# Performance work log

Measured on AMD Instinct MI355X. Metric: run time of the kernel, lower is better.

## Reference

```python
import jax, jax.numpy as jnp
import numpy as np
from jax import lax

B, HS, WS_, DIM = 4, 64, 64, 512
NH, WSZ = 8, 2
WH, SH, HD = 4, 4, 64        # wavelet heads, window heads, head_dim
WDIM, SDIM, RED = 256, 256, 64  # w_dim, s_dim, w_dim//4
SCALE = HD ** -0.5
EPS = 1e-5


def dwt_haar(x):
    # x: [B,C,H,W] -> [B,4C,H/2,W/2]; exact haar 2x2 stride-2 depthwise conv
    a = x[:, :, 0::2, 0::2]; b = x[:, :, 0::2, 1::2]
    c = x[:, :, 1::2, 0::2]; d = x[:, :, 1::2, 1::2]
    ll = 0.5 * (a + b + c + d)
    lh = 0.5 * (a + b - c - d)
    hl = 0.5 * (a - b + c - d)
    hh = 0.5 * (a - b - c + d)
    return jnp.concatenate([ll, lh, hl, hh], axis=1)


def idwt_haar(x):
    # x: [B,4C,h,w] -> [B,C,2h,2w]; exact haar conv_transpose stride 2
    Bx, C4, h, w = x.shape
    C = C4 // 4
    ll, lh, hl, hh = jnp.split(x, 4, axis=1)
    y00 = 0.5 * (ll + lh + hl + hh)
    y01 = 0.5 * (ll + lh - hl - hh)
    y10 = 0.5 * (ll - lh + hl - hh)
    y11 = 0.5 * (ll - lh - hl + hh)
    top = jnp.stack([y00, y01], axis=-1).reshape(Bx, C, h, 2 * w)
    bot = jnp.stack([y10, y11], axis=-1).reshape(Bx, C, h, 2 * w)
    return jnp.stack([top, bot], axis=-2).reshape(Bx, C, 2 * h, 2 * w)


def bn2d(x, g, b):
    # eval-mode BatchNorm2d with running_mean=0, running_var=1
    s = g / jnp.sqrt(1.0 + EPS)
    return x * s[None, :, None, None] + b[None, :, None, None]


def layernorm(x, g, b):
    m = jnp.mean(x, axis=-1, keepdims=True)
    v = jnp.var(x, axis=-1, keepdims=True)
    return (x - m) / jnp.sqrt(v + EPS) * g + b


def wsda_forward(x, wq_w, kv_ln_g, kv_ln_b, wkv_w, wkv_b, wproj_w, wproj_b,
                 reduce_w, reduce_b, reduce_bn_g, reduce_bn_b,
                 filter_w, filter_b, filter_bn_g, filter_bn_b,
                 sqkv_w, sproj_w, sproj_b, H, W):
    Bx, N, C = x.shape
    x4 = x.reshape(Bx, H, W, C)  # ws divides H,W -> no padding

    # ---- windowed attention branch (sa) ----
    hg, wg = H // WSZ, W // WSZ
    G, L = hg * wg, WSZ * WSZ
    xg = x4.reshape(Bx, hg, WSZ, wg, WSZ, C).transpose(0, 1, 3, 2, 4, 5).reshape(Bx, G, L, C)
    qkv = (xg @ sqkv_w).reshape(Bx, G, L, 3, SH, HD)
    q = qkv[:, :, :, 0].transpose(0, 1, 3, 2, 4)  # [B,G,SH,L,HD]
    k = qkv[:, :, :, 1].transpose(0, 1, 3, 2, 4)
    v = qkv[:, :, :, 2].transpose(0, 1, 3, 2, 4)
    attn = jax.nn.softmax(jnp.einsum('bghld,bghmd->bghlm', q, k) * SCALE, axis=-1)
    o = jnp.einsum('bghlm,bghmd->bghld', attn, v)
    o = o.transpose(0, 1, 3, 2, 4).reshape(Bx, hg, wg, WSZ, WSZ, SDIM)
    o = o.transpose(0, 1, 3, 2, 4, 5).reshape(Bx, H, W, SDIM)
    sa_out = o @ sproj_w + sproj_b

    # ---- wavelet attention branch (wa) ----
    q = (x4.reshape(Bx, N, C) @ wq_w).reshape(Bx, N, WH, HD).transpose(0, 2, 1, 3)  # [B,WH,N,HD]
    xc = x4.transpose(0, 3, 1, 2)  # NCHW
    r = jnp.einsum('bchw,co->bohw', xc, reduce_w) + reduce_b[None, :, None, None]
    r = jax.nn.relu(bn2d(r, reduce_bn_g, reduce_bn_b))          # [B,RED,H,W]
    xd = dwt_haar(r)                                            # [B,WDIM,H/2,W/2]
    f = lax.conv_general_dilated(xd, filter_w, (1, 1), 'SAME',
                                 dimension_numbers=('NCHW', 'OIHW', 'NCHW'))
    f = f + filter_b[None, :, None, None]
    xd = jax.nn.relu(bn2d(f, filter_bn_g, filter_bn_b))         # [B,WDIM,H/2,W/2]
    xi = idwt_haar(xd)                                          # [B,RED,H,W]
    x_idwt = xi.reshape(Bx, RED, H * W).transpose(0, 2, 1)      # [B,N,RED]
    kv_in = xd.reshape(Bx, WDIM, -1).transpose(0, 2, 1)         # [B,M,WDIM], M=(H/2)(W/2)
    kv_in = layernorm(kv_in, kv_ln_g, kv_ln_b)
    kv = (kv_in @ wkv_w + wkv_b).reshape(Bx, -1, 2, WH, HD)
    kk = kv[:, :, 0].transpose(0, 2, 1, 3)                      # [B,WH,M,HD]
    vv = kv[:, :, 1].transpose(0, 2, 1, 3)
    attn = jax.nn.softmax(jnp.einsum('bhnd,bhmd->bhnm', q, kk) * SCALE, axis=-1)
    ow = jnp.einsum('bhnm,bhmd->bhnd', attn, vv).transpose(0, 2, 1, 3).reshape(Bx, N, WDIM)
    wa_out = (jnp.concatenate([ow, x_idwt], axis=-1) @ wproj_w + wproj_b).reshape(Bx, H, W, WDIM)

    out = jnp.concatenate([sa_out, wa_out], axis=-1).reshape(Bx, N, C)
    return out


def setup_inputs() -> dict:
    key = jax.random.key(0)
    ks = jax.random.split(key, 10)
    w = lambda k, s: jax.random.normal(k, s, jnp.float32) * 0.02
    return {
        'x': jax.random.normal(ks[0], (B, HS * WS_, DIM), jnp.float32),
        'wq_w': w(ks[1], (DIM, WDIM)),
        'kv_ln_g': jnp.ones((WDIM,), jnp.float32),
        'kv_ln_b': jnp.zeros((WDIM,), jnp.float32),
        'wkv_w': w(ks[2], (WDIM, 2 * WDIM)),
        'wkv_b': jnp.zeros((2 * WDIM,), jnp.float32),
        'wproj_w': w(ks[3], (WDIM + RED, WDIM)),
        'wproj_b': jnp.zeros((WDIM,), jnp.float32),
        'reduce_w': w(ks[4], (DIM, RED)),
        'reduce_b': jnp.zeros((RED,), jnp.float32),
        'reduce_bn_g': jnp.ones((RED,), jnp.float32),
        'reduce_bn_b': jnp.zeros((RED,), jnp.float32),
        'filter_w': w(ks[5], (WDIM, WDIM, 3, 3)),
        'filter_b': jnp.zeros((WDIM,), jnp.float32),
        'filter_bn_g': jnp.ones((WDIM,), jnp.float32),
        'filter_bn_b': jnp.zeros((WDIM,), jnp.float32),
        'sqkv_w': w(ks[6], (DIM, 3 * SDIM)),
        'sproj_w': w(ks[7], (SDIM, SDIM)),
        'sproj_b': jnp.zeros((SDIM,), jnp.float32),
        'H': HS,
        'W': WS_,
    }


def reference(x, wq_w, kv_ln_g, kv_ln_b, wkv_w, wkv_b, wproj_w, wproj_b,
              reduce_w, reduce_b, reduce_bn_g, reduce_bn_b,
              filter_w, filter_b, filter_bn_g, filter_bn_b,
              sqkv_w, sproj_w, sproj_b, H, W):
    return wsda_forward(x, wq_w, kv_ln_g, kv_ln_b, wkv_w, wkv_b, wproj_w, wproj_b,
                        reduce_w, reduce_b, reduce_bn_g, reduce_bn_b,
                        filter_w, filter_b, filter_bn_g, filter_bn_b,
                        sqkv_w, sproj_w, sproj_b, H, W)
```

## Files before the change

kernel.cpp:

```cpp
#include <hip/hip_runtime.h>
#include <hip/hip_bf16.h>
#include <math.h>

#define WEPS 1e-5f
#define WSCALE 0.125f
#define QSCALE 0.1803368801111244f

enum { EPI_NONE=0, EPI_BIAS=1, EPI_BN_RELU=2 };

typedef __attribute__((ext_vector_type(8))) short bf16x8;
typedef __attribute__((ext_vector_type(4))) float f32x4;

static __device__ inline unsigned short f2bf(float f) {
    __hip_bfloat16 h = __float2bfloat16(f);
    return *(unsigned short*)&h;
}
static __device__ inline float exp2_fast(float x) {
    float r;
    asm("v_exp_f32 %0, %1" : "=v"(r) : "v"(x));
    return r;
}
static __device__ inline unsigned cvt_pk_bf16(float a, float b) {
    unsigned r;
    asm("v_cvt_pk_bf16_f32 %0, %1, %2" : "=v"(r) : "v"(a), "v"(b));
    return r;
}
static __device__ inline int xcd_swizzle_id() {
    int id = blockIdx.x;
    int q = gridDim.x >> 3;
    return (id & 7) * q + (id >> 3);
}

static __device__ inline bf16x8 lds_frag(const unsigned short* base, int row, int inner) {
    int byte = row * 128 + (inner ^ ((row & 7) << 4));
    return *(const bf16x8*)((const char*)base + byte);
}
static __device__ inline bf16x8 lds_frag256(const unsigned short* base, int row, int inner) {
    int byte = row * 256 + (inner ^ ((row & 15) << 4));
    return *(const bf16x8*)((const char*)base + byte);
}

template<int EPI, int OBF16>
__launch_bounds__(256)
__global__ void gemm_bf16(const __hip_bfloat16* __restrict__ A, int lda,
                          const __hip_bfloat16* __restrict__ Bt, int K,
                          void* __restrict__ Cv, int ldc, int N, int nbx,
                          const float* __restrict__ bias,
                          const float* __restrict__ bn_g,
                          const float* __restrict__ bn_b,
                          float oscale)
{
    __shared__ unsigned short As[8192];
    __shared__ unsigned short Bs[8192];
    const int tid = threadIdx.x;
    const int lane = tid & 63, wv = tid >> 6;
    const int g = lane >> 4, l16 = lane & 15;
    const int wr = wv >> 1, wc = wv & 1;
    const int w = xcd_swizzle_id();
    const int bm = (w / nbx) << 7;
    const int bn = (w % nbx) << 7;
    f32x4 acc[4][4];
    #pragma unroll
    for (int i = 0; i < 4; i++)
        #pragma unroll
        for (int j = 0; j < 4; j++)
            #pragma unroll
            for (int r = 0; r < 4; r++) acc[i][j][r] = 0.f;

    for (int k0 = 0; k0 < K; k0 += 64) {
        __syncthreads();
        #pragma unroll
        for (int it = 0; it < 4; it++) {
            int idx = tid + (it << 8);
            int row = idx >> 3, seg = idx & 7;
            int wb = row * 128 + ((seg << 4) ^ ((row & 7) << 4));
            float4 av = *(const float4*)(A + (size_t)(bm + row) * lda + k0 + (seg << 3));
            *(float4*)((char*)As + wb) = av;
            int col = bn + row;
            float4 bv = make_float4(0.f,0.f,0.f,0.f);
            if (col < N) bv = *(const float4*)(Bt + (size_t)col * K + k0 + (seg << 3));
            *(float4*)((char*)Bs + wb) = bv;
        }
        __syncthreads();
        #pragma unroll
        for (int ks = 0; ks < 2; ks++) {
            bf16x8 af[4], bfr[4];
            #pragma unroll
            for (int i = 0; i < 4; i++)
                af[i] = lds_frag(As, (wr<<6) + (i<<4) + l16, (ks<<6) + (g<<4));
            #pragma unroll
            for (int j = 0; j < 4; j++)
                bfr[j] = lds_frag(Bs, (wc<<6) + (j<<4) + l16, (ks<<6) + (g<<4));
            #pragma unroll
            for (int i = 0; i < 4; i++)
                #pragma unroll
                for (int j = 0; j < 4; j++)
                    acc[i][j] = __builtin_amdgcn_mfma_f32_16x16x32_bf16(af[i], bfr[j], acc[i][j], 0, 0, 0);
        }
    }
    const float bn_s = 0.99999500003749968f;
    #pragma unroll
    for (int i = 0; i < 4; i++) {
        int m = bm + (wr<<6) + (i<<4) + (g<<2);
        #pragma unroll
        for (int j = 0; j < 4; j++) {
            int c = bn + (wc<<6) + (j<<4) + l16;
            if (c >= N) continue;
            float bi = (EPI != EPI_NONE) ? bias[c] : 0.f;
            float sc = 1.f, bb = 0.f;
            if (EPI == EPI_BN_RELU) { sc = bn_g[c] * bn_s; bb = bn_b[c]; }
            #pragma unroll
            for (int r = 0; r < 4; r++) {
                float t = acc[i][j][r] * oscale + bi;
                if (EPI == EPI_BN_RELU) t = fmaxf(t * sc + bb, 0.f);
                if (OBF16) ((__hip_bfloat16*)Cv)[(size_t)(m+r)*ldc + c] = __float2bfloat16(t);
                else       ((float*)Cv)[(size_t)(m+r)*ldc + c] = t;
            }
        }
    }
}

__launch_bounds__(256)
__global__ void gemmX(const __hip_bfloat16* __restrict__ A,
                      const __hip_bfloat16* __restrict__ Bt,
                      __hip_bfloat16* __restrict__ qkvb,
                      __hip_bfloat16* __restrict__ qbw,
                      float* __restrict__ rbuf,
                      const float* __restrict__ red_b,
                      const float* __restrict__ rbn_g,
                      const float* __restrict__ rbn_b)
{
    __shared__ unsigned short As[8192];
    __shared__ unsigned short Bs[8192];
    const int tid = threadIdx.x;
    const int lane = tid & 63, wv = tid >> 6;
    const int g = lane >> 4, l16 = lane & 15;
    const int wr = wv >> 1, wc = wv & 1;
    const int w = xcd_swizzle_id();
    const int bm = (w / 9) << 7;
    const int bn = (w % 9) << 7;
    f32x4 acc[4][4];
    #pragma unroll
    for (int i = 0; i < 4; i++)
        #pragma unroll
        for (int j = 0; j < 4; j++)
            #pragma unroll
            for (int r = 0; r < 4; r++) acc[i][j][r] = 0.f;

    for (int k0 = 0; k0 < 512; k0 += 64) {
        __syncthreads();
        #pragma unroll
        for (int it = 0; it < 4; it++) {
            int idx = tid + (it << 8);
            int row = idx >> 3, seg = idx & 7;
            int wb = row * 128 + ((seg << 4) ^ ((row & 7) << 4));
            float4 av = *(const float4*)(A + (size_t)(bm + row) * 512 + k0 + (seg << 3));
            *(float4*)((char*)As + wb) = av;
            int col = bn + row;
            float4 bv = make_float4(0.f,0.f,0.f,0.f);
            if (col < 1088) bv = *(const float4*)(Bt + (size_t)col * 512 + k0 + (seg << 3));
            *(float4*)((char*)Bs + wb) = bv;
        }
        __syncthreads();
        #pragma unroll
        for (int ks = 0; ks < 2; ks++) {
            bf16x8 af[4], bfr[4];
            #pragma unroll
            for (int i = 0; i < 4; i++)
                af[i] = lds_frag(As, (wr<<6) + (i<<4) + l16, (ks<<6) + (g<<4));
            #pragma unroll
            for (int j = 0; j < 4; j++)
                bfr[j] = lds_frag(Bs, (wc<<6) + (j<<4) + l16, (ks<<6) + (g<<4));
            #pragma unroll
            for (int i = 0; i < 4; i++)
                #pragma unroll
                for (int j = 0; j < 4; j++)
                    acc[i][j] = __builtin_amdgcn_mfma_f32_16x16x32_bf16(af[i], bfr[j], acc[i][j], 0, 0, 0);
        }
    }
    const float bn_s = 0.99999500003749968f;
    #pragma unroll
    for (int i = 0; i < 4; i++) {
        int m = bm + (wr<<6) + (i<<4) + (g<<2);
        #pragma unroll
        for (int j = 0; j < 4; j++) {
            int c = bn + (wc<<6) + (j<<4) + l16;
            if (c >= 1088) continue;
            if (c < 768) {
                #pragma unroll
                for (int r = 0; r < 4; r++)
                    qkvb[(size_t)(m+r)*768 + c] = __float2bfloat16(acc[i][j][r]);
            } else if (c < 1024) {
                int c2 = c - 768;
                #pragma unroll
                for (int r = 0; r < 4; r++)
                    qbw[(size_t)(m+r)*256 + c2] = __float2bfloat16(acc[i][j][r] * QSCALE);
            } else {
                int c2 = c - 1024;
                float sc = rbn_g[c2] * bn_s, bb = rbn_b[c2], bi = red_b[c2];
                #pragma unroll
                for (int r = 0; r < 4; r++)
                    rbuf[(size_t)(m+r)*64 + c2] = fmaxf((acc[i][j][r] + bi) * sc + bb, 0.f);
            }
        }
    }
}

__launch_bounds__(256)
__global__ void gemm64_kv(const __hip_bfloat16* __restrict__ A,
                          const __hip_bfloat16* __restrict__ Bt,
                          __hip_bfloat16* __restrict__ kbo,
                          __hip_bfloat16* __restrict__ vto,
                          const float* __restrict__ bias)
{
    __shared__ unsigned short As[2][4096];
    __shared__ unsigned short Bs[2][4096];
    const int tid = threadIdx.x;
    const int lane = tid & 63, wv = tid >> 6;
    const int g = lane >> 4, l16 = lane & 15;
    const int wr = wv >> 1, wc = wv & 1;
    const int bm = blockIdx.y << 6;
    const int bn = blockIdx.x << 6;

    int swb[2];
    const __hip_bfloat16 *Ap[2], *Bp[2];
    #pragma unroll
    for (int it = 0; it < 2; it++) {
        int idx = tid + (it << 8);
        int row = idx >> 3, seg = idx & 7;
        swb[it] = row * 128 + ((seg << 4) ^ ((row & 7) << 4));
        Ap[it] = A  + (size_t)(bm + row) * 256 + (seg << 3);
        Bp[it] = Bt + (size_t)(bn + row) * 256 + (seg << 3);
    }
    f32x4 acc[2][2];
    #pragma unroll
    for (int i = 0; i < 2; i++)
        #pragma unroll
        for (int j = 0; j < 2; j++)
            #pragma unroll
            for (int r = 0; r < 4; r++) acc[i][j][r] = 0.f;

    #pragma unroll
    for (int it = 0; it < 2; it++) {
        *(float4*)((char*)As[0] + swb[it]) = *(const float4*)(Ap[it]);
        *(float4*)((char*)Bs[0] + swb[it]) = *(const float4*)(Bp[it]);
    }
    __syncthreads();

    int cur = 0;
    for (int t = 0; t < 4; t++) {
        float4 ra[2], rb[2];
        const bool has_next = (t < 3);
        if (has_next) {
            #pragma unroll
            for (int it = 0; it < 2; it++) {
                ra[it] = *(const float4*)(Ap[it] + ((t + 1) << 6));
                rb[it] = *(const float4*)(Bp[it] + ((t + 1) << 6));
            }
        }
        #pragma unroll
        for (int ks = 0; ks < 2; ks++) {
            bf16x8 af[2], bfr[2];
            #pragma unroll
            for (int i = 0; i < 2; i++)
                af[i] = lds_frag(As[cur], (wr<<5) + (i<<4) + l16, (ks<<6) + (g<<4));
            #pragma unroll
            for (int j = 0; j < 2; j++)
                bfr[j] = lds_frag(Bs[cur], (wc<<5) + (j<<4) + l16, (ks<<6) + (g<<4));
            #pragma unroll
            for (int i = 0; i < 2; i++)
                #pragma unroll
                for (int j = 0; j < 2; j++)
                    acc[i][j] = __builtin_amdgcn_mfma_f32_16x16x32_bf16(af[i], bfr[j], acc[i][j], 0, 0, 0);
        }
        if (has_next) {
            #pragma unroll
            for (int it = 0; it < 2; it++) {
                *(float4*)((char*)As[cur^1] + swb[it]) = ra[it];
                *(float4*)((char*)Bs[cur^1] + swb[it]) = rb[it];
            }
        }
        __syncthreads();
        cur ^= 1;
    }

    #pragma unroll
    for (int i = 0; i < 2; i++) {
        int m = bm + (wr<<5) + (i<<4) + (g<<2);
        int bimg = m >> 10, tkn0 = m & 1023;
        #pragma unroll
        for (int j = 0; j < 2; j++) {
            int c = bn + (wc<<5) + (j<<4) + l16;
            if (c < 256) {
                int wh = c >> 6, d0 = c & 63;
                __hip_bfloat16* kp = kbo + (((size_t)((bimg<<2)+wh)) << 16) + (size_t)tkn0*64 + d0;
                #pragma unroll
                for (int r = 0; r < 4; r++)
                    kp[r*64] = __float2bfloat16(acc[i][j][r] + bias[c]);
            } else {
                int c2 = c - 256;
                int wh = c2 >> 6, d = c2 & 63;
                float bi = bias[256 + c2];
                ushort4 h;
                h.x = f2bf(acc[i][j][0] + bi);
                h.y = f2bf(acc[i][j][1] + bi);
                h.z = f2bf(acc[i][j][2] + bi);
                h.w = f2bf(acc[i][j][3] + bi);
                *(ushort4*)(vto + (((size_t)((bimg<<2)+wh)) << 16) + (size_t)d*1024 + tkn0) = h;
            }
        }
    }
}

__launch_bounds__(256)
__global__ void gemm_wproj(const __hip_bfloat16* __restrict__ A1,
                           const __hip_bfloat16* __restrict__ A2,
                           const __hip_bfloat16* __restrict__ Bt,
                           float* __restrict__ C,
                           const float* __restrict__ bias)
{
    __shared__ unsigned short As[8192];
    __shared__ unsigned short Bs[8192];
    const int tid = threadIdx.x;
    const int lane = tid & 63, wv = tid >> 6;
    const int g = lane >> 4, l16 = lane & 15;
    const int wr = wv >> 1, wc = wv & 1;
    const int w = xcd_swizzle_id();
    const int bm = (w >> 1) << 7;
    const int bn = (w & 1) << 7;
    f32x4 acc[4][4];
    #pragma unroll
    for (int i = 0; i < 4; i++)
        #pragma unroll
        for (int j = 0; j < 4; j++)
            #pragma unroll
            for (int r = 0; r < 4; r++) acc[i][j][r] = 0.f;

    for (int k0 = 0; k0 < 320; k0 += 64) {
        __syncthreads();
        #pragma unroll
        for (int it = 0; it < 4; it++) {
            int idx = tid + (it << 8);
            int row = idx >> 3, seg = idx & 7;
            int wb = row * 128 + ((seg << 4) ^ ((row & 7) << 4));
            float4 av;
            if (k0 < 256)
                av = *(const float4*)(A1 + (size_t)(bm + row) * 256 + k0 + (seg << 3));
            else
                av = *(const float4*)(A2 + (size_t)(bm + row) * 64 + (k0 - 256) + (seg << 3));
            *(float4*)((char*)As + wb) = av;
            float4 bv = *(const float4*)(Bt + (size_t)(bn + row) * 320 + k0 + (seg << 3));
            *(float4*)((char*)Bs + wb) = bv;
        }
        __syncthreads();
        #pragma unroll
        for (int ks = 0; ks < 2; ks++) {
            bf16x8 af[4], bfr[4];
            #pragma unroll
            for (int i = 0; i < 4; i++)
                af[i] = lds_frag(As, (wr<<6) + (i<<4) + l16, (ks<<6) + (g<<4));
            #pragma unroll
            for (int j = 0; j < 4; j++)
                bfr[j] = lds_frag(Bs, (wc<<6) + (j<<4) + l16, (ks<<6) + (g<<4));
            #pragma unroll
            for (int i = 0; i < 4; i++)
                #pragma unroll
                for (int j = 0; j < 4; j++)
                    acc[i][j] = __builtin_amdgcn_mfma_f32_16x16x32_bf16(af[i], bfr[j], acc[i][j], 0, 0, 0);
        }
    }
    #pragma unroll
    for (int i = 0; i < 4; i++) {
        int m = bm + (wr<<6) + (i<<4) + (g<<2);
        #pragma unroll
        for (int j = 0; j < 4; j++) {
            int c = bn + (wc<<6) + (j<<4) + l16;
            float bi = bias[c];
            #pragma unroll
            for (int r = 0; r < 4; r++)
                C[(size_t)(m+r)*512 + c] = acc[i][j][r] + bi;
        }
    }
}

__launch_bounds__(256)
__global__ void conv3_mfma(const __hip_bfloat16* __restrict__ Xd,
                           const __hip_bfloat16* __restrict__ Wt,
                           float* __restrict__ C,
                           const float* __restrict__ bias,
                           const float* __restrict__ bn_g,
                           const float* __restrict__ bn_b)
{
    __shared__ unsigned short As[2][8192];
    __shared__ unsigned short Bs[2][8192];
    const int tid = threadIdx.x;
    const int lane = tid & 63, wv = tid >> 6;
    const int g = lane >> 4, l16 = lane & 15;
    const int wr = wv >> 1, wc = wv & 1;
    const int bm = blockIdx.y << 6;
    const int bn = blockIdx.x << 6;

    int srow[4], sseg[4], swb[4];
    #pragma unroll
    for (int it = 0; it < 4; it++) {
        int idx = tid + (it << 8);
        srow[it] = idx >> 4;
        sseg[it] = idx & 15;
        swb[it]  = srow[it] * 256 + ((sseg[it] << 4) ^ ((srow[it] & 15) << 4));
    }
    int abase[4], ay[4], ax[4];
    #pragma unroll
    for (int it = 0; it < 4; it++) {
        int m = bm + srow[it];
        int bimg = m >> 10, s = m & 1023;
        ay[it] = s >> 5; ax[it] = s & 31;
        abase[it] = bimg << 10;
    }

    f32x4 acc[2][2];
    #pragma unroll
    for (int i = 0; i < 2; i++)
        #pragma unroll
        for (int j = 0; j < 2; j++)
            #pragma unroll
            for (int r = 0; r < 4; r++) acc[i][j][r] = 0.f;

    #pragma unroll
    for (int it = 0; it < 4; it++) {
        int y = ay[it] - 1, xx = ax[it] - 1;
        float4 av = make_float4(0.f,0.f,0.f,0.f);
        if ((unsigned)y < 32u && (unsigned)xx < 32u)
            av = *(const float4*)(Xd + ((size_t)(abase[it] + (y<<5) + xx) << 8) + (sseg[it] << 3));
        *(float4*)((char*)As[0] + swb[it]) = av;
        float4 bv = *(const float4*)(Wt + (size_t)(bn + srow[it]) * 2304 + (sseg[it] << 3));
        *(float4*)((char*)Bs[0] + swb[it]) = bv;
    }
    __syncthreads();

    int cur = 0;
    for (int t = 0; t < 18; t++) {
        float4 ra[4], rb[4];
        const bool has_next = (t + 1 < 18);
        if (has_next) {
            int tn = t + 1;
            int tap = tn >> 1;
            int dy = tap / 3 - 1;
            int dx = tap - (tap / 3) * 3 - 1;
            int i0 = (tn & 1) << 7;
            #pragma unroll
            for (int it = 0; it < 4; it++) {
                int y = ay[it] + dy, xx = ax[it] + dx;
                ra[it] = make_float4(0.f,0.f,0.f,0.f);
                if ((unsigned)y < 32u && (unsigned)xx < 32u)
                    ra[it] = *(const float4*)(Xd + ((size_t)(abase[it] + (y<<5) + xx) << 8) + i0 + (sseg[it] << 3));
                rb[it] = *(const float4*)(Wt + (size_t)(bn + srow[it]) * 2304 + tn * 128 + (sseg[it] << 3));
            }
        }
        #pragma unroll
        for (int ks = 0; ks < 4; ks++) {
            bf16x8 af[2], bfr[2];
            #pragma unroll
            for (int i = 0; i < 2; i++)
                af[i] = lds_frag256(As[cur], (wr<<5) + (i<<4) + l16, (ks<<6) + (g<<4));
            #pragma unroll
            for (int j = 0; j < 2; j++)
                bfr[j] = lds_frag256(Bs[cur], (wc<<5) + (j<<4) + l16, (ks<<6) + (g<<4));
            #pragma unroll
            for (int i = 0; i < 2; i++)
                #pragma unroll
                for (int j = 0; j < 2; j++)
                    acc[i][j] = __builtin_amdgcn_mfma_f32_16x16x32_bf16(af[i], bfr[j], acc[i][j], 0, 0, 0);
        }
        if (has_next) {
            #pragma unroll
            for (int it = 0; it < 4; it++) {
                *(float4*)((char*)As[cur^1] + swb[it]) = ra[it];
                *(float4*)((char*)Bs[cur^1] + swb[it]) = rb[it];
            }
        }
        __syncthreads();
        cur ^= 1;
    }

    const float bn_s = 0.99999500003749968f;
    #pragma unroll
    for (int i = 0; i < 2; i++) {
        int m = bm + (wr<<5) + (i<<4) + (g<<2);
        #pragma unroll
        for (int j = 0; j < 2; j++) {
            int c = bn + (wc<<5) + (j<<4) + l16;
            float sc = bn_g[c] * bn_s, bb = bn_b[c], bi = bias[c];
            #pragma unroll
            for (int r = 0; r < 4; r++)
                C[(size_t)(m + r) * 256 + c] = fmaxf((acc[i][j][r] + bi) * sc + bb, 0.f);
        }
    }
}

static __device__ inline void tr_task(const float* in, __hip_bfloat16* o,
                                      int K, int N, int nb, int tid)
{
    int idx = nb * 256 + tid;
    int n = idx / K, k = idx - n * K;
    o[idx] = __float2bfloat16(in[(size_t)k * N + n]);
}

__global__ void prep_all(const float* __restrict__ x,
                         const float* __restrict__ sqkv_w, const float* __restrict__ wq_w,
                         const float* __restrict__ reduce_w, const float* __restrict__ sproj_w,
                         const float* __restrict__ wkv_w, const float* __restrict__ wproj_w,
                         const float* __restrict__ filter_w,
                         __hip_bfloat16* __restrict__ xb, __hip_bfloat16* __restrict__ sqkvT,
                         __hip_bfloat16* __restrict__ wqT, __hip_bfloat16* __restrict__ redT,
                         __hip_bfloat16* __restrict__ sprojT, __hip_bfloat16* __restrict__ wkvT,
                         __hip_bfloat16* __restrict__ wprojT, __hip_bfloat16* __restrict__ wt2b)
{
    int bid = blockIdx.x, tid = threadIdx.x;
    if (bid < 8192) {
        int i = bid * 256 + tid;
        float4 v = ((const float4*)x)[i];
        ushort4 h;
        h.x = f2bf(v.x); h.y = f2bf(v.y); h.z = f2bf(v.z); h.w = f2bf(v.w);
        *(ushort4*)(xb + (size_t)i * 4) = h;
        return;
    }
    bid -= 8192;
    if (bid < 1536) { tr_task(sqkv_w, sqkvT, 512, 768, bid, tid); return; }
    bid -= 1536;
    if (bid < 512)  { tr_task(wq_w, wqT, 512, 256, bid, tid); return; }
    bid -= 512;
    if (bid < 128)  { tr_task(reduce_w, redT, 512, 64, bid, tid); return; }
    bid -= 128;
    if (bid < 256)  { tr_task(sproj_w, sprojT, 256, 256, bid, tid); return; }
    bid -= 256;
    if (bid < 512)  { tr_task(wkv_w, wkvT, 256, 512, bid, tid); return; }
    bid -= 512;
    if (bid < 320)  { tr_task(wproj_w, wprojT, 320, 256, bid, tid); return; }
    bid -= 320;
    {
        int oc = bid;
        const float* src = filter_w + (size_t)(oc * 256 + tid) * 9;
        __hip_bfloat16* dst = wt2b + (size_t)oc * 2304 + tid;
        #pragma unroll
        for (int tap = 0; tap < 9; tap++)
            dst[tap * 256] = __float2bfloat16(src[tap]);
    }
}

__launch_bounds__(256)
__global__ void win_attn(const __hip_bfloat16* __restrict__ qkv,
                         __hip_bfloat16* __restrict__ sa_o)
{
    int gw = blockIdx.x * 4 + (threadIdx.x >> 6);
    int lane = threadIdx.x & 63;
    int b  = gw >> 12;
    int g  = (gw >> 2) & 1023;
    int sh = gw & 3;
    int hg = g >> 5, wg = g & 31;
    float q[4], k[4], v[4];
    int rows[4];
    #pragma unroll
    for (int l = 0; l < 4; l++) {
        int h = (hg << 1) + (l >> 1), w = (wg << 1) + (l & 1);
        int row = (b << 12) + (h << 6) + w;
        rows[l] = row;
        const __hip_bfloat16* p = qkv + (size_t)row * 768 + sh * 64 + lane;
        q[l] = __bfloat162float(p[0]);
        k[l] = __bfloat162float(p[256]);
        v[l] = __bfloat162float(p[512]);
    }
    float s[4][4];
    #pragma unroll
    for (int l = 0; l < 4; l++)
        #pragma unroll
        for (int m = 0; m < 4; m++) s[l][m] = q[l] * k[m];
    #pragma unroll
    for (int off = 32; off > 0; off >>= 1)
        #pragma unroll
        for (int l = 0; l < 4; l++)
            #pragma unroll
            for (int m = 0; m < 4; m++)
                s[l][m] += __shfl_xor(s[l][m], off, 64);
    #pragma unroll
    for (int l = 0; l < 4; l++) {
        float s0 = s[l][0]*WSCALE, s1 = s[l][1]*WSCALE, s2 = s[l][2]*WSCALE, s3 = s[l][3]*WSCALE;
        float mx = fmaxf(fmaxf(s0,s1), fmaxf(s2,s3));
        float p0 = __expf(s0-mx), p1 = __expf(s1-mx), p2 = __expf(s2-mx), p3 = __expf(s3-mx);
        float inv = 1.f / (p0+p1+p2+p3);
        float o = (p0*v[0] + p1*v[1] + p2*v[2] + p3*v[3]) * inv;
        sa_o[(size_t)rows[l] * 256 + sh * 64 + lane] = __float2bfloat16(o);
    }
}

__global__ void dwt_kernel(const float* __restrict__ r, __hip_bfloat16* __restrict__ xd)
{
    int t = blockIdx.x * 256 + threadIdx.x;
    int o = t & 63;
    int x = (t >> 6) & 31;
    int y = (t >> 11) & 31;
    int b = t >> 16;
    const float* rb = r + (b << 18);
    int base = ((y << 1) << 6) + (x << 1);
    float a  = rb[(base     ) * 64 + o];
    float bb = rb[(base +  1) * 64 + o];
    float c  = rb[(base + 64) * 64 + o];
    float d  = rb[(base + 65) * 64 + o];
    float ll = 0.5f*(a+bb+c+d), lh = 0.5f*(a+bb-c-d);
    float hl = 0.5f*(a-bb+c-d), hh = 0.5f*(a-bb-c+d);
    __hip_bfloat16* outp = xd + (((b << 10) + (y << 5) + x) << 8) + o;
    outp[0]   = __float2bfloat16(ll);
    outp[64]  = __float2bfloat16(lh);
    outp[128] = __float2bfloat16(hl);
    outp[192] = __float2bfloat16(hh);
}

__launch_bounds__(256)
__global__ void ln_idwt(const float* __restrict__ X, const float* __restrict__ g,
                        const float* __restrict__ bta, __hip_bfloat16* __restrict__ Y,
                        __hip_bfloat16* __restrict__ xi)
{
    int bid = blockIdx.x;
    int t = threadIdx.x;
    if (bid < 4096) {
        int row = bid;
        float x = X[(size_t)row * 256 + t];
        __shared__ float red[4];
        int wv = t >> 6, ln = t & 63;
        float s = x;
        #pragma unroll
        for (int off = 32; off > 0; off >>= 1) s += __shfl_xor(s, off, 64);
        if (ln == 0) red[wv] = s;
        __syncthreads();
        float m = (red[0]+red[1]+red[2]+red[3]) * (1.f/256.f);
        float d = x - m;
        float s2 = d * d;
        #pragma unroll
        for (int off = 32; off > 0; off >>= 1) s2 += __shfl_xor(s2, off, 64);
        __syncthreads();
        if (ln == 0) red[wv] = s2;
        __syncthreads();
        float var = (red[0]+red[1]+red[2]+red[3]) * (1.f/256.f);
        float inv = 1.f / sqrtf(var + WEPS);
        Y[(size_t)row * 256 + t] = __float2bfloat16(d * inv * g[t] + bta[t]);
        return;
    }
    int tt = (bid - 4096) * 256 + t;
    int o = tt & 63;
    int x = (tt >> 6) & 31;
    int y = (tt >> 11) & 31;
    int b = tt >> 16;
    const float* p = X + (((b << 10) + (y << 5) + x) << 8);
    float ll = p[o], lh = p[64+o], hl = p[128+o], hh = p[192+o];
    float y00 = 0.5f*(ll+lh+hl+hh);
    float y01 = 0.5f*(ll+lh-hl-hh);
    float y10 = 0.5f*(ll-lh+hl-hh);
    float y11 = 0.5f*(ll-lh-hl+hh);
    __hip_bfloat16* ob = xi + ((size_t)b << 18);
    int base = ((y << 1) << 6) + (x << 1);
    ob[(size_t)(base     ) * 64 + o] = __float2bfloat16(y00);
    ob[(size_t)(base +  1) * 64 + o] = __float2bfloat16(y01);
    ob[(size_t)(base + 64) * 64 + o] = __float2bfloat16(y10);
    ob[(size_t)(base + 65) * 64 + o] = __float2bfloat16(y11);
}

__launch_bounds__(256)
__global__ void flash_mfma(const __hip_bfloat16* __restrict__ qb,
                           const __hip_bfloat16* __restrict__ kb,
                           const __hip_bfloat16* __restrict__ vt,
                           __hip_bfloat16* __restrict__ ow)
{
    __shared__ unsigned short Ks[4096];
    __shared__ unsigned short Vs[4096];
    const int tid = threadIdx.x;
    const int wv = tid >> 6;
    const int lane = tid & 63;
    const int g = lane >> 4, q16 = lane & 15;
    const int bh = blockIdx.y;
    const int b = bh >> 2, wh = bh & 3;
    const int qbase = (blockIdx.x << 6) + (wv << 4);

    const __hip_bfloat16* qp = qb + ((size_t)((b << 12) + qbase + q16)) * 256 + wh * 64 + g * 8;
    bf16x8 qf0 = *(const bf16x8*)qp;
    bf16x8 qf1 = *(const bf16x8*)(qp + 32);

    const __hip_bfloat16* kbase = kb + ((size_t)bh << 16);
    const __hip_bfloat16* vbase = vt + ((size_t)bh << 16);

    f32x4 oacc[4];
    #pragma unroll
    for (int dc = 0; dc < 4; dc++)
        #pragma unroll
        for (int r = 0; r < 4; r++) oacc[dc][r] = 0.f;
    float m_cur = -1e30f;
    float lsum_part = 0.f;

    for (int t0 = 0; t0 < 1024; t0 += 64) {
        __syncthreads();
        #pragma unroll
        for (int it = 0; it < 2; it++) {
            int off = (tid << 4) + (it << 12);
            int row = off >> 7;
            int inner = off & 127;
            int wb = row * 128 + (inner ^ ((row & 7) << 4));
            float4 kd = *(const float4*)(kbase + (t0 + row) * 64 + (inner >> 1));
            float4 vd = *(const float4*)(vbase + row * 1024 + t0 + (inner >> 1));
            *(float4*)((char*)Ks + wb) = kd;
            *(float4*)((char*)Vs + wb) = vd;
        }
        __syncthreads();

        f32x4 st[4];
        __builtin_amdgcn_s_setprio(1);
        #pragma unroll
        for (int sub = 0; sub < 4; sub++) {
            #pragma unroll
            for (int r = 0; r < 4; r++) st[sub][r] = 0.f;
            bf16x8 k0 = lds_frag(Ks, sub * 16 + q16, g * 16);
            bf16x8 k1 = lds_frag(Ks, sub * 16 + q16, 64 + g * 16);
            st[sub] = __builtin_amdgcn_mfma_f32_16x16x32_bf16(k0, qf0, st[sub], 0, 0, 0);
            st[sub] = __builtin_amdgcn_mfma_f32_16x16x32_bf16(k1, qf1, st[sub], 0, 0, 0);
        }
        __builtin_amdgcn_s_setprio(0);

        float pmax = -1e30f;
        #pragma unroll
        for (int t = 0; t < 4; t++)
            #pragma unroll
            for (int r = 0; r < 4; r++) pmax = fmaxf(pmax, st[t][r]);
        if (!__all(pmax <= m_cur + 11.5f)) {
            float mx = pmax;
            mx = fmaxf(mx, __shfl_xor(mx, 16, 64));
            mx = fmaxf(mx, __shfl_xor(mx, 32, 64));
            float m_new = fmaxf(m_cur, mx);
            float alpha = exp2_fast(m_cur - m_new);
            lsum_part *= alpha;
            #pragma unroll
            for (int r = 0; r < 4; r++) {
                float sc = __shfl(alpha, (g << 2) + r, 64);
                #pragma unroll
                for (int dc = 0; dc < 4; dc++) oacc[dc][r] *= sc;
            }
            m_cur = m_new;
        }

        float psum = 0.f;
        unsigned pk[4][2];
        #pragma unroll
        for (int t = 0; t < 4; t++) {
            float p0 = exp2_fast(st[t][0] - m_cur), p1 = exp2_fast(st[t][1] - m_cur);
            float p2 = exp2_fast(st[t][2] - m_cur), p3 = exp2_fast(st[t][3] - m_cur);
            psum += (p0 + p1) + (p2 + p3);
            pk[t][0] = cvt_pk_bf16(p0, p1);
            pk[t][1] = cvt_pk_bf16(p2, p3);
        }
        lsum_part += psum;

        bool ghi = (g & 2) != 0;
        unsigned pkA0[2], pkA1[2];
        pkA0[0] = ghi ? pk[1][0] : pk[0][0];
        pkA0[1] = ghi ? pk[1][1] : pk[0][1];
        pkA1[0] = ghi ? pk[3][0] : pk[2][0];
        pkA1[1] = ghi ? pk[3][1] : pk[2][1];
        union { int u[4]; bf16x8 v; } A0, A1;
        #pragma unroll
        for (int c = 0; c < 4; c++) {
            int src = (((2 * g + (c >> 1)) & 3) << 4) | q16;
            A0.u[c] = __shfl((int)pkA0[c & 1], src, 64);
            A1.u[c] = __shfl((int)pkA1[c & 1], src, 64);
        }

        __builtin_amdgcn_s_setprio(1);
        #pragma unroll
        for (int dc = 0; dc < 4; dc++) {
            bf16x8 v0 = lds_frag(Vs, dc * 16 + q16, g * 16);
            bf16x8 v1 = lds_frag(Vs, dc * 16 + q16, 64 + g * 16);
            oacc[dc] = __builtin_amdgcn_mfma_f32_16x16x32_bf16(A0.v, v0, oacc[dc], 0, 0, 0);
            oacc[dc] = __builtin_amdgcn_mfma_f32_16x16x32_bf16(A1.v, v1, oacc[dc], 0, 0, 0);
        }
        __builtin_amdgcn_s_setprio(0);
    }

    lsum_part += __shfl_xor(lsum_part, 16, 64);
    lsum_part += __shfl_xor(lsum_part, 32, 64);
    #pragma unroll
    for (int r = 0; r < 4; r++) {
        float inv = 1.f / __shfl(lsum_part, (g << 2) + r, 64);
        int qrow = (b << 12) + qbase + (g << 2) + r;
        #pragma unroll
        for (int dc = 0; dc < 4; dc++)
            ow[(size_t)qrow * 256 + wh * 64 + dc * 16 + q16] =
                __float2bfloat16(oacc[dc][r] * inv);
    }
}

extern "C" void kernel_launch(void* const* d_in, const int* in_sizes, int n_in,
                              void* d_out, int out_size, void* d_ws, size_t ws_size,
                              hipStream_t stream)
{
    const float* x        = (const float*)d_in[0];
    const float* wq_w     = (const float*)d_in[1];
    const float* kv_ln_g  = (const float*)d_in[2];
    const float* kv_ln_b  = (const float*)d_in[3];
    const float* wkv_w    = (const float*)d_in[4];
    const float* wkv_b    = (const float*)d_in[5];
    const float* wproj_w  = (const float*)d_in[6];
    const float* wproj_b  = (const float*)d_in[7];
    const float* reduce_w = (const float*)d_in[8];
    const float* reduce_b = (const float*)d_in[9];
    const float* rbn_g    = (const float*)d_in[10];
    const float* rbn_b    = (const float*)d_in[11];
    const float* filter_w = (const float*)d_in[12];
    const float* filter_b = (const float*)d_in[13];
    const float* fbn_g    = (const float*)d_in[14];
    const float* fbn_b    = (const float*)d_in[15];
    const float* sqkv_w   = (const float*)d_in[16];
    const float* sproj_w  = (const float*)d_in[17];
    const float* sproj_b  = (const float*)d_in[18];
    float* out = (float*)d_out;
    float* ws  = (float*)d_ws;

    __hip_bfloat16* qkvb  = (__hip_bfloat16*)(ws);
    __hip_bfloat16* owb   = (__hip_bfloat16*)(ws);
    __hip_bfloat16* sa_ob = (__hip_bfloat16*)(ws + 6291456);
    __hip_bfloat16* xb    = (__hip_bfloat16*)(ws + 8388608);
    __hip_bfloat16* sqkvT = (__hip_bfloat16*)(ws + 12582912);
    __hip_bfloat16* wqT   = (__hip_bfloat16*)(ws + 12779520);
    __hip_bfloat16* redT  = (__hip_bfloat16*)(ws + 12845056);
    __hip_bfloat16* sprojT= (__hip_bfloat16*)(ws + 12861440);
    __hip_bfloat16* wkvT  = (__hip_bfloat16*)(ws + 12894208);
    __hip_bfloat16* wprojT= (__hip_bfloat16*)(ws + 13025280);
    __hip_bfloat16* wt2b  = (__hip_bfloat16*)(ws + 13066240);
    float* rbuf  = ws + 13361152;
    __hip_bfloat16* xd1b  = (__hip_bfloat16*)(ws + 14409728);
    float* xd2   = ws + 14934016;
    __hip_bfloat16* kvinb = (__hip_bfloat16*)(ws + 15982592);
    __hip_bfloat16* xidwtb= (__hip_bfloat16*)(ws + 16506880);
    __hip_bfloat16* qbw   = (__hip_bfloat16*)(ws + 17031168);
    __hip_bfloat16* kbb   = (__hip_bfloat16*)(ws + 19128320);
    __hip_bfloat16* vtb   = (__hip_bfloat16*)(ws + 19652608);

    dim3 blk(256);

    prep_all<<<dim3(11712), blk, 0, stream>>>(x, sqkv_w, wq_w, reduce_w, sproj_w,
                                              wkv_w, wproj_w, filter_w,
                                              xb, sqkvT, wqT, redT, sprojT, wkvT,
                                              wprojT, wt2b);

    gemmX<<<dim3(1152), blk, 0, stream>>>(xb, sqkvT, qkvb, qbw, rbuf,
                                          reduce_b, rbn_g, rbn_b);
    win_attn<<<dim3(4096), blk, 0, stream>>>(qkvb, sa_ob);
    gemm_bf16<EPI_BIAS,0><<<dim3(256), blk, 0, stream>>>(sa_ob, 256, sprojT, 256, out, 512,
                                                         256, 2, sproj_b, nullptr, nullptr, 1.f);
    dwt_kernel<<<dim3(1024), blk, 0, stream>>>(rbuf, xd1b);
    conv3_mfma<<<dim3(4,64), blk, 0, stream>>>(xd1b, wt2b, xd2, filter_b, fbn_g, fbn_b);
    ln_idwt<<<dim3(5120), blk, 0, stream>>>(xd2, kv_ln_g, kv_ln_b, kvinb, xidwtb);
    gemm64_kv<<<dim3(8,64), blk, 0, stream>>>(kvinb, wkvT, kbb, vtb, wkv_b);
    flash_mfma<<<dim3(64,16), blk, 0, stream>>>(qbw, kbb, vtb, owb);
    gemm_wproj<<<dim3(256), blk, 0, stream>>>(owb, xidwtb, wprojT, out + 256, wproj_b);
}
```

Before: 177.8 us.

## Double-buffer LDS tiles with register prefetch in three GEMM kernels

Converts the generic GEMM, the fused QKV GEMM and the wproj GEMM from single-buffered LDS staging to a double-buffered ping-pong scheme. The next K-tile is loaded from global memory into registers before the MFMA loop over the current tile, then written to the other LDS buffer, which removes one barrier per iteration and lets global load latency overlap compute. Per-thread address math is also hoisted out of the loop. The cost is doubled LDS use (64KB per block) and more live registers, which may reduce occupancy.

```diff
diff --git a/kernel.cpp b/kernel.cpp
--- a/kernel.cpp
+++ b/kernel.cpp
@@ -50,8 +50,8 @@
                           const float* __restrict__ bn_b,
                           float oscale)
 {
-    __shared__ unsigned short As[8192];
-    __shared__ unsigned short Bs[8192];
+    __shared__ unsigned short As[2][8192];
+    __shared__ unsigned short Bs[2][8192];
     const int tid = threadIdx.x;
     const int lane = tid & 63, wv = tid >> 6;
     const int g = lane >> 4, l16 = lane & 15;
@@ -59,6 +59,20 @@
     const int w = xcd_swizzle_id();
     const int bm = (w / nbx) << 7;
     const int bn = (w % nbx) << 7;
+
+    int swb[4];
+    const __hip_bfloat16 *Ap[4], *Bp[4];
+    bool bok[4];
+    #pragma unroll
+    for (int it = 0; it < 4; it++) {
+        int idx = tid + (it << 8);
+        int row = idx >> 3, seg = idx & 7;
+        swb[it] = row * 128 + ((seg << 4) ^ ((row & 7) << 4));
+        Ap[it] = A + (size_t)(bm + row) * lda + (seg << 3);
+        int col = bn + row;
+        bok[it] = col < N;
+        Bp[it] = Bt + (size_t)(bok[it] ? col : 0) * K + (seg << 3);
+    }
     f32x4 acc[4][4];
     #pragma unroll
     for (int i = 0; i < 4; i++)
@@ -67,36 +81,53 @@
             #pragma unroll
             for (int r = 0; r < 4; r++) acc[i][j][r] = 0.f;
 
-    for (int k0 = 0; k0 < K; k0 += 64) {
-        __syncthreads();
-        #pragma unroll
-        for (int it = 0; it < 4; it++) {
-            int idx = tid + (it << 8);
-            int row = idx >> 3, seg = idx & 7;
-            int wb = row * 128 + ((seg << 4) ^ ((row & 7) << 4));
-            float4 av = *(const float4*)(A + (size_t)(bm + row) * lda + k0 + (seg << 3));
-            *(float4*)((char*)As + wb) = av;
-            int col = bn + row;
-            float4 bv = make_float4(0.f,0.f,0.f,0.f);
-            if (col < N) bv = *(const float4*)(Bt + (size_t)col * K + k0 + (seg << 3));
-            *(float4*)((char*)Bs + wb) = bv;
-        }
-        __syncthreads();
+    #pragma unroll
+    for (int it = 0; it < 4; it++) {
+        *(float4*)((char*)As[0] + swb[it]) = *(const float4*)(Ap[it]);
+        float4 bv = make_float4(0.f,0.f,0.f,0.f);
+        if (bok[it]) bv = *(const float4*)(Bp[it]);
+        *(float4*)((char*)Bs[0] + swb[it]) = bv;
+    }
+    __syncthreads();
+
+    int cur = 0;
+    const int niter = K >> 6;
+    for (int t = 0; t < niter; t++) {
+        float4 ra[4], rb[4];
+        const bool has_next = (t + 1 < niter);
+        if (has_next) {
+            int kb = (t + 1) << 6;
+            #pragma unroll
+            for (int it = 0; it < 4; it++) {
+                ra[it] = *(const float4*)(Ap[it] + kb);
+                rb[it] = make_float4(0.f,0.f,0.f,0.f);
+                if (bok[it]) rb[it] = *(const float4*)(Bp[it] + kb);
+            }
+        }
         #pragma unroll
         for (int ks = 0; ks < 2; ks++) {
             bf16x8 af[4], bfr[4];
             #pragma unroll
             for (int i = 0; i < 4; i++)
-                af[i] = lds_frag(As, (wr<<6) + (i<<4) + l16, (ks<<6) + (g<<4));
+                af[i] = lds_frag(As[cur], (wr<<6) + (i<<4) + l16, (ks<<6) + (g<<4));
             #pragma unroll
             for (int j = 0; j < 4; j++)
-                bfr[j] = lds_frag(Bs, (wc<<6) + (j<<4) + l16, (ks<<6) + (g<<4));
+                bfr[j] = lds_frag(Bs[cur], (wc<<6) + (j<<4) + l16, (ks<<6) + (g<<4));
             #pragma unroll
             for (int i = 0; i < 4; i++)
                 #pragma unroll
                 for (int j = 0; j < 4; j++)
                     acc[i][j] = __builtin_amdgcn_mfma_f32_16x16x32_bf16(af[i], bfr[j], acc[i][j], 0, 0, 0);
         }
+        if (has_next) {
+            #pragma unroll
+            for (int it = 0; it < 4; it++) {
+                *(float4*)((char*)As[cur^1] + swb[it]) = ra[it];
+                *(float4*)((char*)Bs[cur^1] + swb[it]) = rb[it];
+            }
+        }
+        __syncthreads();
+        cur ^= 1;
     }
     const float bn_s = 0.99999500003749968f;
     #pragma unroll
@@ -130,8 +161,8 @@
                       const float* __restrict__ rbn_g,
                       const float* __restrict__ rbn_b)
 {
-    __shared__ unsigned short As[8192];
-    __shared__ unsigned short Bs[8192];
+    __shared__ unsigned short As[2][8192];
+    __shared__ unsigned short Bs[2][8192];
     const int tid = threadIdx.x;
     const int lane = tid & 63, wv = tid >> 6;
     const int g = lane >> 4, l16 = lane & 15;
@@ -139,6 +170,20 @@
     const int w = xcd_swizzle_id();
     const int bm = (w / 9) << 7;
     const int bn = (w % 9) << 7;
+
+    int swb[4];
+    const __hip_bfloat16 *Ap[4], *Bp[4];
+    bool bok[4];
+    #pragma unroll
+    for (int it = 0; it < 4; it++) {
+        int idx = tid + (it << 8);
+        int row = idx >> 3, seg = idx & 7;
+        swb[it] = row * 128 + ((seg << 4) ^ ((row & 7) << 4));
+        Ap[it] = A + (size_t)(bm + row) * 512 + (seg << 3);
+        int col = bn + row;
+        bok[it] = col < 1088;
+        Bp[it] = Bt + (size_t)(bok[it] ? col : 0) * 512 + (seg << 3);
+    }
     f32x4 acc[4][4];
     #pragma unroll
     for (int i = 0; i < 4; i++)
@@ -147,36 +192,52 @@
             #pragma unroll
             for (int r = 0; r < 4; r++) acc[i][j][r] = 0.f;
 
-    for (int k0 = 0; k0 < 512; k0 += 64) {
-        __syncthreads();
-        #pragma unroll
-        for (int it = 0; it < 4; it++) {
-            int idx = tid + (it << 8);
-            int row = idx >> 3, seg = idx & 7;
-            int wb = row * 128 + ((seg << 4) ^ ((row & 7) << 4));
-            float4 av = *(const float4*)(A + (size_t)(bm + row) * 512 + k0 + (seg << 3));
-            *(float4*)((char*)As + wb) = av;
-            int col = bn + row;
-            float4 bv = make_float4(0.f,0.f,0.f,0.f);
-            if (col < 1088) bv = *(const float4*)(Bt + (size_t)col * 512 + k0 + (seg << 3));
-            *(float4*)((char*)Bs + wb) = bv;
-        }
-        __syncthreads();
+    #pragma unroll
+    for (int it = 0; it < 4; it++) {
+        *(float4*)((char*)As[0] + swb[it]) = *(const float4*)(Ap[it]);
+        float4 bv = make_float4(0.f,0.f,0.f,0.f);
+        if (bok[it]) bv = *(const float4*)(Bp[it]);
+        *(float4*)((char*)Bs[0] + swb[it]) = bv;
+    }
+    __syncthreads();
+
+    int cur = 0;
+    for (int t = 0; t < 8; t++) {
+        float4 ra[4], rb[4];
+        const bool has_next = (t < 7);
+        if (has_next) {
+            int kb = (t + 1) << 6;
+            #pragma unroll
+            for (int it = 0; it < 4; it++) {
+                ra[it] = *(const float4*)(Ap[it] + kb);
+                rb[it] = make_float4(0.f,0.f,0.f,0.f);
+                if (bok[it]) rb[it] = *(const float4*)(Bp[it] + kb);
+            }
+        }
         #pragma unroll
         for (int ks = 0; ks < 2; ks++) {
             bf16x8 af[4], bfr[4];
             #pragma unroll
             for (int i = 0; i < 4; i++)
-                af[i] = lds_frag(As, (wr<<6) + (i<<4) + l16, (ks<<6) + (g<<4));
+                af[i] = lds_frag(As[cur], (wr<<6) + (i<<4) + l16, (ks<<6) + (g<<4));
             #pragma unroll
             for (int j = 0; j < 4; j++)
-                bfr[j] = lds_frag(Bs, (wc<<6) + (j<<4) + l16, (ks<<6) + (g<<4));
+                bfr[j] = lds_frag(Bs[cur], (wc<<6) + (j<<4) + l16, (ks<<6) + (g<<4));
             #pragma unroll
             for (int i = 0; i < 4; i++)
                 #pragma unroll
                 for (int j = 0; j < 4; j++)
                     acc[i][j] = __builtin_amdgcn_mfma_f32_16x16x32_bf16(af[i], bfr[j], acc[i][j], 0, 0, 0);
         }
+        if (has_next) {
+            #pragma unroll
+            for (int it = 0; it < 4; it++) {
+                *(float4*)((char*)As[cur^1] + swb[it]) = ra[it];
+                *(float4*)((char*)Bs[cur^1] + swb[it]) = rb[it];
+            }
+        }
+        __syncthreads();
+        cur ^= 1;
     }
     const float bn_s = 0.99999500003749968f;
     #pragma unroll
@@ -319,8 +380,8 @@
                            float* __restrict__ C,
                            const float* __restrict__ bias)
 {
-    __shared__ unsigned short As[8192];
-    __shared__ unsigned short Bs[8192];
+    __shared__ unsigned short As[2][8192];
+    __shared__ unsigned short Bs[2][8192];
     const int tid = threadIdx.x;
     const int lane = tid & 63, wv = tid >> 6;
     const int g = lane >> 4, l16 = lane & 15;
@@ -328,6 +389,16 @@
     const int w = xcd_swizzle_id();
     const int bm = (w >> 1) << 7;
     const int bn = (w & 1) << 7;
+
+    int srow[4], sseg[4], swb[4];
+    const __hip_bfloat16 *Bp[4];
+    #pragma unroll
+    for (int it = 0; it < 4; it++) {
+        int idx = tid + (it << 8);
+        srow[it] = idx >> 3; sseg[it] = idx & 7;
+        swb[it] = srow[it] * 128 + ((sseg[it] << 4) ^ ((srow[it] & 7) << 4));
+        Bp[it] = Bt + (size_t)(bn + srow[it]) * 320 + (sseg[it] << 3);
+    }
     f32x4 acc[4][4];
     #pragma unroll
     for (int i = 0; i < 4; i++)
@@ -336,38 +407,53 @@
             #pragma unroll
             for (int r = 0; r < 4; r++) acc[i][j][r] = 0.f;
 
-    for (int k0 = 0; k0 < 320; k0 += 64) {
-        __syncthreads();
-        #pragma unroll
-        for (int it = 0; it < 4; it++) {
-            int idx = tid + (it << 8);
-            int row = idx >> 3, seg = idx & 7;
-            int wb = row * 128 + ((seg << 4) ^ ((row & 7) << 4));
-            float4 av;
-            if (k0 < 256)
-                av = *(const float4*)(A1 + (size_t)(bm + row) * 256 + k0 + (seg << 3));
-            else
-                av = *(const float4*)(A2 + (size_t)(bm + row) * 64 + (k0 - 256) + (seg << 3));
-            *(float4*)((char*)As + wb) = av;
-            float4 bv = *(const float4*)(Bt + (size_t)(bn + row) * 320 + k0 + (seg << 3));
-            *(float4*)((char*)Bs + wb) = bv;
-        }
-        __syncthreads();
+    #pragma unroll
+    for (int it = 0; it < 4; it++) {
+        *(float4*)((char*)As[0] + swb[it]) =
+            *(const float4*)(A1 + (size_t)(bm + srow[it]) * 256 + (sseg[it] << 3));
+        *(float4*)((char*)Bs[0] + swb[it]) = *(const float4*)(Bp[it]);
+    }
+    __syncthreads();
+
+    int cur = 0;
+    for (int t = 0; t < 5; t++) {
+        float4 ra[4], rb[4];
+        const bool has_next = (t < 4);
+        if (has_next) {
+            int kb = (t + 1) << 6;
+            #pragma unroll
+            for (int it = 0; it < 4; it++) {
+                if (kb < 256)
+                    ra[it] = *(const float4*)(A1 + (size_t)(bm + srow[it]) * 256 + kb + (sseg[it] << 3));
+                else
+                    ra[it] = *(const float4*)(A2 + (size_t)(bm + srow[it]) * 64 + (kb - 256) + (sseg[it] << 3));
+                rb[it] = *(const float4*)(Bp[it] + kb);
+            }
+        }
         #pragma unroll
         for (int ks = 0; ks < 2; ks++) {
             bf16x8 af[4], bfr[4];
             #pragma unroll
             for (int i = 0; i < 4; i++)
-                af[i] = lds_frag(As, (wr<<6) + (i<<4) + l16, (ks<<6) + (g<<4));
+                af[i] = lds_frag(As[cur], (wr<<6) + (i<<4) + l16, (ks<<6) + (g<<4));
             #pragma unroll
             for (int j = 0; j < 4; j++)
-                bfr[j] = lds_frag(Bs, (wc<<6) + (j<<4) + l16, (ks<<6) + (g<<4));
+                bfr[j] = lds_frag(Bs[cur], (wc<<6) + (j<<4) + l16, (ks<<6) + (g<<4));
             #pragma unroll
             for (int i = 0; i < 4; i++)
                 #pragma unroll
                 for (int j = 0; j < 4; j++)
                     acc[i][j] = __builtin_amdgcn_mfma_f32_16x16x32_bf16(af[i], bfr[j], acc[i][j], 0, 0, 0);
         }
+        if (has_next) {
+            #pragma unroll
+            for (int it = 0; it < 4; it++) {
+                *(float4*)((char*)As[cur^1] + swb[it]) = ra[it];
+                *(float4*)((char*)Bs[cur^1] + swb[it]) = rb[it];
+            }
+        }
+        __syncthreads();
+        cur ^= 1;
     }
     #pragma unroll
     for (int i = 0; i < 4; i++) {
```

Measured after the change: 207.3 us. +16.6%, slower.

## Double-buffer shared memory tiles in gemmX with register prefetch

Applied to the files above, without the earlier changes.

The input projection GEMM now uses two LDS buffers for A and B. The next K-tile is prefetched into registers while MFMAs run on the current tile, then written into the alternate buffer, which leaves one barrier per iteration instead of two. Global load addresses are precomputed once. The aim is to hide global memory latency behind compute, at the cost of doubled LDS use (64KB) and more registers, which may reduce occupancy.

```diff
diff --git a/kernel.cpp b/kernel.cpp
--- a/kernel.cpp
+++ b/kernel.cpp
@@ -130,8 +130,8 @@
                       const float* __restrict__ rbn_g,
                       const float* __restrict__ rbn_b)
 {
-    __shared__ unsigned short As[8192];
-    __shared__ unsigned short Bs[8192];
+    __shared__ unsigned short As[2][8192];
+    __shared__ unsigned short Bs[2][8192];
     const int tid = threadIdx.x;
     const int lane = tid & 63, wv = tid >> 6;
     const int g = lane >> 4, l16 = lane & 15;
@@ -139,6 +139,20 @@
     const int w = xcd_swizzle_id();
     const int bm = (w / 9) << 7;
     const int bn = (w % 9) << 7;
+
+    int swb[4];
+    const __hip_bfloat16 *Ap[4], *Bp[4];
+    bool bok[4];
+    #pragma unroll
+    for (int it = 0; it < 4; it++) {
+        int idx = tid + (it << 8);
+        int row = idx >> 3, seg = idx & 7;
+        swb[it] = row * 128 + ((seg << 4) ^ ((row & 7) << 4));
+        Ap[it] = A + (size_t)(bm + row) * 512 + (seg << 3);
+        int col = bn + row;
+        bok[it] = col < 1088;
+        Bp[it] = Bt + (size_t)(bok[it] ? col : 0) * 512 + (seg << 3);
+    }
     f32x4 acc[4][4];
     #pragma unroll
     for (int i = 0; i < 4; i++)
@@ -147,36 +161,52 @@
             #pragma unroll
             for (int r = 0; r < 4; r++) acc[i][j][r] = 0.f;
 
-    for (int k0 = 0; k0 < 512; k0 += 64) {
-        __syncthreads();
-        #pragma unroll
-        for (int it = 0; it < 4; it++) {
-            int idx = tid + (it << 8);
-            int row = idx >> 3, seg = idx & 7;
-            int wb = row * 128 + ((seg << 4) ^ ((row & 7) << 4));
-            float4 av = *(const float4*)(A + (size_t)(bm + row) * 512 + k0 + (seg << 3));
-            *(float4*)((char*)As + wb) = av;
-            int col = bn + row;
-            float4 bv = make_float4(0.f,0.f,0.f,0.f);
-            if (col < 1088) bv = *(const float4*)(Bt + (size_t)col * 512 + k0 + (seg << 3));
-            *(float4*)((char*)Bs + wb) = bv;
-        }
-        __syncthreads();
+    #pragma unroll
+    for (int it = 0; it < 4; it++) {
+        *(float4*)((char*)As[0] + swb[it]) = *(const float4*)(Ap[it]);
+        float4 bv = make_float4(0.f,0.f,0.f,0.f);
+        if (bok[it]) bv = *(const float4*)(Bp[it]);
+        *(float4*)((char*)Bs[0] + swb[it]) = bv;
+    }
+    __syncthreads();
+
+    int cur = 0;
+    for (int t = 0; t < 8; t++) {
+        float4 ra[4], rb[4];
+        const bool has_next = (t < 7);
+        if (has_next) {
+            int kb = (t + 1) << 6;
+            #pragma unroll
+            for (int it = 0; it < 4; it++) {
+                ra[it] = *(const float4*)(Ap[it] + kb);
+                rb[it] = make_float4(0.f,0.f,0.f,0.f);
+                if (bok[it]) rb[it] = *(const float4*)(Bp[it] + kb);
+            }
+        }
         #pragma unroll
         for (int ks = 0; ks < 2; ks++) {
             bf16x8 af[4], bfr[4];
             #pragma unroll
             for (int i = 0; i < 4; i++)
-                af[i] = lds_frag(As, (wr<<6) + (i<<4) + l16, (ks<<6) + (g<<4));
+                af[i] = lds_frag(As[cur], (wr<<6) + (i<<4) + l16, (ks<<6) + (g<<4));
             #pragma unroll
             for (int j = 0; j < 4; j++)
-                bfr[j] = lds_frag(Bs, (wc<<6) + (j<<4) + l16, (ks<<6) + (g<<4));
+                bfr[j] = lds_frag(Bs[cur], (wc<<6) + (j<<4) + l16, (ks<<6) + (g<<4));
             #pragma unroll
             for (int i = 0; i < 4; i++)
                 #pragma unroll
                 for (int j = 0; j < 4; j++)
                     acc[i][j] = __builtin_amdgcn_mfma_f32_16x16x32_bf16(af[i], bfr[j], acc[i][j], 0, 0, 0);
         }
+        if (has_next) {
+            #pragma unroll
+            for (int it = 0; it < 4; it++) {
+                *(float4*)((char*)As[cur^1] + swb[it]) = ra[it];
+                *(float4*)((char*)Bs[cur^1] + swb[it]) = rb[it];
+            }
+        }
+        __syncthreads();
+        cur ^= 1;
     }
     const float bn_s = 0.99999500003749968f;
     #pragma unroll
```

After: 159.2 us. -10.5%, faster.
